# Performance work log

Measured on AMD Instinct MI355X. Metric: run time of the kernel, lower is better.

Reference implementation:

```python
import jax, jax.numpy as jnp
import numpy as np

B, T, E, H, O = 32, 512, 768, 3132, 19


def _ln(x, g, b, eps=1e-5):
    m = x.mean(-1, keepdims=True)
    v = x.var(-1, keepdims=True)
    return (x - m) / jnp.sqrt(v + eps) * g + b


def _cell(x, h, wih, bih, whh, bhh):
    # torch.nn.RNNCell with tanh nonlinearity
    return jnp.tanh(x @ wih.T + bih + h @ whh.T + bhh)


def _mha(seq, wqkv, bqkv, wo, bo):
    # seq: [T,B,D]; single-head torch MultiheadAttention (eval mode, no dropout)
    D = seq.shape[-1]
    qkv = seq @ wqkv.T + bqkv
    q, k, v = jnp.split(qkv, 3, axis=-1)
    scores = jnp.einsum('tbd,sbd->bts', q, k) / jnp.sqrt(jnp.asarray(D, seq.dtype))
    a = jax.nn.softmax(scores, axis=-1)
    ctx = jnp.einsum('bts,sbd->tbd', a, v)
    return ctx @ wo.T + bo


def setup_inputs() -> dict:
    key = jax.random.key(0)
    ks = jax.random.split(key, 12)
    s = lambda k, shape: jax.random.normal(k, shape, jnp.float32) * 0.02
    return {
        'x': jax.random.normal(ks[0], (B, T, E), jnp.float32),
        'in_g': jnp.ones((E,), jnp.float32), 'in_b': jnp.zeros((E,), jnp.float32),
        'w_ih1': s(ks[1], (H, E)), 'w_hh1': s(ks[2], (H, H)),
        'b_ih1': jnp.zeros((H,), jnp.float32), 'b_hh1': jnp.zeros((H,), jnp.float32),
        'ln1_g': jnp.ones((H,), jnp.float32), 'ln1_b': jnp.zeros((H,), jnp.float32),
        'w_ih2': s(ks[3], (E, H)), 'w_hh2': s(ks[4], (E, E)),
        'b_ih2': jnp.zeros((E,), jnp.float32), 'b_hh2': jnp.zeros((E,), jnp.float32),
        'mha1_wqkv': s(ks[5], (3 * H, H)), 'mha1_bqkv': jnp.zeros((3 * H,), jnp.float32),
        'mha1_wo': s(ks[6], (H, H)), 'mha1_bo': jnp.zeros((H,), jnp.float32),
        'mha2_wqkv': s(ks[7], (3 * E, E)), 'mha2_bqkv': jnp.zeros((3 * E,), jnp.float32),
        'mha2_wo': s(ks[8], (E, E)), 'mha2_bo': jnp.zeros((E,), jnp.float32),
        'w_cls': s(ks[9], (O, E)), 'b_cls': jnp.zeros((O,), jnp.float32),
    }


def reference(x, in_g, in_b, w_ih1, w_hh1, b_ih1, b_hh1, ln1_g, ln1_b,
              w_ih2, w_hh2, b_ih2, b_hh2,
              mha1_wqkv, mha1_bqkv, mha1_wo, mha1_bo,
              mha2_wqkv, mha2_bqkv, mha2_wo, mha2_bo, w_cls, b_cls):
    b = x.shape[0]
    xn = _ln(x, in_g, in_b)            # input_norm
    xs = jnp.swapaxes(xn, 0, 1)        # [T,B,E]
    h1_0 = jnp.zeros((b, w_ih1.shape[0]), x.dtype)
    h2_0 = jnp.zeros((b, w_ih2.shape[0]), x.dtype)

    def step(carry, xt):
        h1, h2 = carry
        h1 = _ln(_cell(xt, h1, w_ih1, b_ih1, w_hh1, b_hh1), ln1_g, ln1_b)
        h2 = _cell(h1, h2, w_ih2, b_ih2, w_hh2, b_hh2)
        return (h1, h2), (h1, h2)

    _, (h1s, h2s) = jax.lax.scan(step, (h1_0, h2_0), xs)  # [T,B,H], [T,B,E]
    ctx1 = _mha(h1s, mha1_wqkv, mha1_bqkv, mha1_wo, mha1_bo)  # dropout is identity in eval
    ctx2 = _mha(h2s, mha2_wqkv, mha2_bqkv, mha2_wo, mha2_bo)
    # the original second loop overwrites h1/h2 each t; only t = T-1 survives
    h1 = _cell(xs[-1], ctx1[-1], w_ih1, b_ih1, w_hh1, b_hh1)
    h2 = _cell(h1, ctx2[-1], w_ih2, b_ih2, w_hh2, b_hh2)
    return h2 @ w_cls.T + b_cls
```

## Files before the change

### kernel.cpp

```cpp
#include <hip/hip_runtime.h>
#include <cstdint>
#include <cmath>

#define BB 32
#define TT 512
#define EE 768
#define HH 3132
#define HP 3136
#define OO 19

#define NBLK 451
#define NTHR 256
#define WP 456
#define AP 232


#define PT(t) (((t) * 331) & 511)

typedef __attribute__((ext_vector_type(8))) short s8v;
typedef __attribute__((ext_vector_type(4))) float f4v;
typedef __attribute__((ext_vector_type(8))) unsigned short u16x8;

__device__ __forceinline__ unsigned short f2bf(float f) {
    uint32_t u = __float_as_uint(f);
    uint32_t r = u + 0x7FFFu + ((u >> 16) & 1u);
    return (unsigned short)(r >> 16);
}
__device__ __forceinline__ float bf2f(unsigned short h) {
    return __uint_as_float(((uint32_t)h) << 16);
}

#define MFMA(a, b, c) __builtin_amdgcn_mfma_f32_16x16x32_bf16((a), (b), (c), 0, 0, 0)

__device__ __forceinline__ f4v ld4_sc(const void* p) {
    f4v v;
    asm volatile("global_load_dwordx4 %0, %1, off sc0 sc1" : "=v"(v) : "v"(p) : "memory");
    return v;
}
#define WAITV() do { asm volatile("s_waitcnt vmcnt(0)" ::: "memory"); \
                     __builtin_amdgcn_sched_barrier(0); } while (0)
__device__ __forceinline__ void st_sc(float* p, float v) {
    __hip_atomic_store(p, v, __ATOMIC_RELAXED, __HIP_MEMORY_SCOPE_AGENT);
}
__device__ __forceinline__ void st16_sc(void* p, u16x8 v) {
    asm volatile("global_store_dwordx4 %0, %1, off sc0 sc1" :: "v"(p), "v"(v) : "memory");
}
__device__ __forceinline__ void st8_sc(void* p, uint2 v) {
    asm volatile("global_store_dwordx2 %0, %1, off sc0 sc1" :: "v"(p), "v"(v) : "memory");
}

struct PP {
    const unsigned short *xw1hi, *xw1lo;
    const unsigned short *whh1hi, *whh1lo, *wih2, *whh2;
    const float *b1c, *b2c, *gpad, *bepad;
    unsigned short *h1hist, *h2hist;
    unsigned short *h1nlo, *h2lo;
    float *part1, *part2;
    unsigned int *grp;
    unsigned int *epoch;
};

__device__ __forceinline__ void gbar(const PP& p, unsigned int k) {
    __syncthreads();
    asm volatile("s_waitcnt vmcnt(0)" ::: "memory");
    if (threadIdx.x == 0)
        __hip_atomic_fetch_add(&p.grp[(blockIdx.x & 63) * 32], 1u,
                               __ATOMIC_RELAXED, __HIP_MEMORY_SCOPE_AGENT);
    if (blockIdx.x == 0) {
        if (threadIdx.x < 64) {
            unsigned int mem = 7u + (threadIdx.x < (NBLK & 63) ? 1u : 0u);
            unsigned int tgt = mem * k;
            long g = 0;
            while (__hip_atomic_load(&p.grp[threadIdx.x * 32], __ATOMIC_RELAXED,
                                     __HIP_MEMORY_SCOPE_AGENT) < tgt) {
                __builtin_amdgcn_s_sleep(2);
                if (++g > (1L << 16)) break;
            }
        }
        __syncthreads();
        if (threadIdx.x == 0)
            __hip_atomic_store(p.epoch, k, __ATOMIC_RELAXED, __HIP_MEMORY_SCOPE_AGENT);
    } else {
        if (threadIdx.x == 0) {
            long g = 0;
            while (__hip_atomic_load(p.epoch, __ATOMIC_RELAXED,
                                     __HIP_MEMORY_SCOPE_AGENT) < k) {
                __builtin_amdgcn_s_sleep(2);
                if (++g > (1L << 16)) break;
            }
        }
    }
    __syncthreads();
    asm volatile("" ::: "memory");
}

__global__ __launch_bounds__(NTHR, 2) void persist_k(PP p) {
    __shared__ unsigned short Wlds[64][WP];
    __shared__ unsigned short Alds[32][AP];
    __shared__ float redS[4], redQ[4];
    const int blk = blockIdx.x, tid = threadIdx.x;
    const int wid = tid >> 6, lane = tid & 63;
    const int r = lane & 15, kg = lane >> 4;
    unsigned int bar = 0;

    const int t1nt = blk / 7,          t1ks = blk % 7;
    const int t2i  = blk - 343,        t2nt = t2i / 7, t2ks = t2i % 7;
    const int t3i  = blk - 427,        t3nt = t3i / 2, t3kh = t3i % 2;

    if (blk < 343) {
        const unsigned short* src = p.whh1hi + (size_t)(t1nt * 64) * HP + t1ks * 448;
        #pragma unroll
        for (int i = 0; i < 14; ++i) {
            int idx = tid + i * 256;
            int row = idx / 56, c8 = idx % 56;
            *(uint4*)&Wlds[row][c8 * 8] = *(const uint4*)(src + (size_t)row * HP + c8 * 8);
        }
    } else if (blk < 427) {
        const unsigned short* src = p.wih2 + (size_t)(t2nt * 64) * HP + t2ks * 448;
        #pragma unroll
        for (int i = 0; i < 14; ++i) {
            int idx = tid + i * 256;
            int row = idx / 56, c8 = idx % 56;
            *(uint4*)&Wlds[row][c8 * 8] = *(const uint4*)(src + (size_t)row * HP + c8 * 8);
        }
    } else {
        const unsigned short* src = p.whh2 + (size_t)(t3nt * 64) * EE + t3kh * 384;
        #pragma unroll
        for (int i = 0; i < 12; ++i) {
            int idx = tid + i * 256;
            int row = idx / 48, c8 = idx % 48;
            *(uint4*)&Wlds[row][c8 * 8] = *(const uint4*)(src + (size_t)row * EE + c8 * 8);
        }
    }
    __syncthreads();

    for (int t = 0; t <= TT; ++t) {
        if (blk < 343) {
            if (t >= 1 && t <= TT - 1) {
                f4v a0 = {0.f,0.f,0.f,0.f}, a1 = {0.f,0.f,0.f,0.f};
                const unsigned short* Wl = p.whh1lo + (size_t)(t1nt * 64 + wid * 16 + r) * HP + t1ks * 448 + kg * 8;
                const unsigned short* ringb = p.h1hist + (size_t)PT(t - 1) * BB * HP + t1ks * 448 + kg * 8;
                for (int hx = 0; hx < 2; ++hx) {
                    __syncthreads();
                    {
                        f4v lv[4];
                        #pragma unroll
                        for (int i = 0; i < 4; ++i) {
                            int idx = tid + i * 256;
                            int row = (idx < 896) ? idx / 28 : 0;
                            int c8  = (idx < 896) ? idx % 28 : 0;
                            lv[i] = ld4_sc(p.h1nlo + (size_t)row * HP + t1ks * 448 + hx * 224 + c8 * 8);
                        }
                        WAITV();
                        #pragma unroll
                        for (int i = 0; i < 4; ++i) {
                            int idx = tid + i * 256;
                            if (idx < 896) {
                                int row = idx / 28, c8 = idx % 28;
                                *(f4v*)&Alds[row][c8 * 8] = lv[i];
                            }
                        }
                    }
                    __syncthreads();
                    const unsigned short* Ah0 = ringb + (size_t)r * HP + hx * 224;
                    const unsigned short* Ah1 = ringb + (size_t)(r + 16) * HP + hx * 224;
                    const unsigned short* Wlh = Wl + hx * 224;
                    #pragma unroll
                    for (int kb = 0; kb < 7; ++kb) {
                        s8v bh  = *(const s8v*)&Wlds[wid * 16 + r][hx * 224 + kb * 32 + kg * 8];
                        s8v bl  = *(const s8v*)(Wlh + kb * 32);
                        s8v ah0 = *(const s8v*)(Ah0 + kb * 32);
                        s8v ah1 = *(const s8v*)(Ah1 + kb * 32);
                        s8v al0 = *(const s8v*)&Alds[r][kb * 32 + kg * 8];
                        s8v al1 = *(const s8v*)&Alds[r + 16][kb * 32 + kg * 8];
                        a0 = MFMA(ah0, bh, a0); a1 = MFMA(ah1, bh, a1);
                        a0 = MFMA(al0, bh, a0); a1 = MFMA(al1, bh, a1);
                        a0 = MFMA(ah0, bl, a0); a1 = MFMA(ah1, bl, a1);
                    }
                }
                int ncol = t1nt * 64 + wid * 16 + r;
                float* pp1 = p.part1 + (size_t)t1ks * BB * HP + ncol;
                #pragma unroll
                for (int q = 0; q < 4; ++q) {
                    st_sc(pp1 + (size_t)(kg * 4 + q) * HP,      a0[q]);
                    st_sc(pp1 + (size_t)(kg * 4 + q + 16) * HP, a1[q]);
                }
            }
        } else if (blk < 427) {
            if (t >= 1) {
                const unsigned short* ringb = p.h1hist + (size_t)PT(t - 1) * BB * HP + t2ks * 448 + kg * 8;
                const unsigned short* Ah0 = ringb + (size_t)r * HP;
                const unsigned short* Ah1 = ringb + (size_t)(r + 16) * HP;
                f4v a0 = {0.f,0.f,0.f,0.f}, a1 = {0.f,0.f,0.f,0.f};
                #pragma unroll
                for (int kb = 0; kb < 14; ++kb) {
                    s8v bh  = *(const s8v*)&Wlds[wid * 16 + r][kb * 32 + kg * 8];
                    s8v ah0 = *(const s8v*)(Ah0 + kb * 32);
                    s8v ah1 = *(const s8v*)(Ah1 + kb * 32);
                    a0 = MFMA(ah0, bh, a0); a1 = MFMA(ah1, bh, a1);
                }
                int ncol = t2nt * 64 + wid * 16 + r;
                float* pp2 = p.part2 + (size_t)t2ks * BB * EE + ncol;
                #pragma unroll
                for (int q = 0; q < 4; ++q) {
                    st_sc(pp2 + (size_t)(kg * 4 + q) * EE,      a0[q]);
                    st_sc(pp2 + (size_t)(kg * 4 + q + 16) * EE, a1[q]);
                }
            }
        } else {
            if (t >= 2) {
                const unsigned short* Hh = p.h2hist + (size_t)PT(t - 2) * BB * EE + t3kh * 384 + kg * 8;
                const unsigned short* Hl = p.h2lo + t3kh * 384 + kg * 8;
                f4v a0 = {0.f,0.f,0.f,0.f}, a1 = {0.f,0.f,0.f,0.f};
                #pragma unroll
                for (int c = 0; c < 2; ++c) {
                    f4v v0l[6], v1l[6];
                    #pragma unroll
                    for (int u = 0; u < 6; ++u) {
                        int kb = c * 6 + u;
                        v0l[u] = ld4_sc(Hl + (size_t)r * EE + kb * 32);
                        v1l[u] = ld4_sc(Hl + (size_t)(r + 16) * EE + kb * 32);
                    }
                    WAITV();
                    #pragma unroll
                    for (int u = 0; u < 6; ++u) {
                        int kb = c * 6 + u;
                        s8v bh  = *(const s8v*)&Wlds[wid * 16 + r][kb * 32 + kg * 8];
                        s8v ah0 = *(const s8v*)(Hh + (size_t)r * EE + kb * 32);
                        s8v ah1 = *(const s8v*)(Hh + (size_t)(r + 16) * EE + kb * 32);
                        a0 = MFMA(ah0, bh, a0);
                        a0 = MFMA(__builtin_bit_cast(s8v, v0l[u]), bh, a0);
                        a1 = MFMA(ah1, bh, a1);
                        a1 = MFMA(__builtin_bit_cast(s8v, v1l[u]), bh, a1);
                    }
                }
                int ncol = t3nt * 64 + wid * 16 + r;
                float* pp2 = p.part2 + (size_t)(7 + t3kh) * BB * EE + ncol;
                #pragma unroll
                for (int q = 0; q < 4; ++q) {
                    st_sc(pp2 + (size_t)(kg * 4 + q) * EE,      a0[q]);
                    st_sc(pp2 + (size_t)(kg * 4 + q + 16) * EE, a1[q]);
                }
            }
        }
        gbar(p, ++bar);

        if (blk < 32) {
            if (t <= TT - 1) {
                const int b = blk;
                const int nb = tid * 16;
                const bool act = (tid < 196);
                float acc[16];
                float s = 0.f, s2 = 0.f;
                if (act) {
                    #pragma unroll
                    for (int k4 = 0; k4 < 4; ++k4) {
                        f4v bb = *(const f4v*)(p.b1c + nb + k4 * 4);
                        #pragma unroll
                        for (int e = 0; e < 4; ++e) acc[k4 * 4 + e] = bb[e];
                    }
                    const u16x8* xh = (const u16x8*)(p.xw1hi + ((size_t)t * BB + b) * HP + nb);
                    const u16x8* xl = (const u16x8*)(p.xw1lo + ((size_t)t * BB + b) * HP + nb);
                    u16x8 h0v = xh[0], h1v = xh[1], l0v = xl[0], l1v = xl[1];
                    #pragma unroll
                    for (int j = 0; j < 8; ++j) acc[j]     += bf2f(h0v[j]) + bf2f(l0v[j]);
                    #pragma unroll
                    for (int j = 0; j < 8; ++j) acc[8 + j] += bf2f(h1v[j]) + bf2f(l1v[j]);
                    if (t > 0) {
                        {
                            f4v tmp[16];
                            #pragma unroll
                            for (int sl = 0; sl < 4; ++sl) {
                                const float* base = p.part1 + ((size_t)sl * BB + b) * HP + nb;
                                #pragma unroll
                                for (int k4 = 0; k4 < 4; ++k4) tmp[sl * 4 + k4] = ld4_sc(base + k4 * 4);
                            }
                            WAITV();
                            #pragma unroll
                            for (int sl = 0; sl < 4; ++sl)
                                #pragma unroll
                                for (int k4 = 0; k4 < 4; ++k4)
                                    #pragma unroll
                                    for (int e = 0; e < 4; ++e) acc[k4 * 4 + e] += tmp[sl * 4 + k4][e];
                        }
                        {
                            f4v tmp[12];
                            #pragma unroll
                            for (int sl = 0; sl < 3; ++sl) {
                                const float* base = p.part1 + ((size_t)(sl + 4) * BB + b) * HP + nb;
                                #pragma unroll
                                for (int k4 = 0; k4 < 4; ++k4) tmp[sl * 4 + k4] = ld4_sc(base + k4 * 4);
                            }
                            WAITV();
                            #pragma unroll
                            for (int sl = 0; sl < 3; ++sl)
                                #pragma unroll
                                for (int k4 = 0; k4 < 4; ++k4)
                                    #pragma unroll
                                    for (int e = 0; e < 4; ++e) acc[k4 * 4 + e] += tmp[sl * 4 + k4][e];
                        }
                    }
                    #pragma unroll
                    for (int j = 0; j < 16; ++j) {
                        if (nb + j < HH) {
                            float v = tanhf(acc[j]);
                            acc[j] = v; s += v; s2 += v * v;
                        } else acc[j] = 0.f;
                    }
                }
                for (int o = 32; o; o >>= 1) { s += __shfl_xor(s, o); s2 += __shfl_xor(s2, o); }
                if (lane == 0) { redS[wid] = s; redQ[wid] = s2; }
                __syncthreads();
                float S  = redS[0] + redS[1] + redS[2] + redS[3];
                float S2 = redQ[0] + redQ[1] + redQ[2] + redQ[3];
                float mm = S / (float)HH;
                float inv = rsqrtf(S2 / (float)HH - mm * mm + 1e-5f);
                __syncthreads();
                if (act) {
                    u16x8 ho0, ho1, lo0, lo1;
                    #pragma unroll
                    for (int k4 = 0; k4 < 4; ++k4) {
                        f4v gv = *(const f4v*)(p.gpad + nb + k4 * 4);
                        f4v bv = *(const f4v*)(p.bepad + nb + k4 * 4);
                        #pragma unroll
                        for (int e = 0; e < 4; ++e) {
                            int j = k4 * 4 + e, n = nb + j;
                            float o = (n < HH) ? (acc[j] - mm) * inv * gv[e] + bv[e] : 0.f;
                            unsigned short hb = f2bf(o);
                            unsigned short lb = f2bf(o - bf2f(hb));
                            if (j < 8) { ho0[j] = hb; lo0[j] = lb; }
                            else       { ho1[j - 8] = hb; lo1[j - 8] = lb; }
                        }
                    }
                    unsigned short* dh = p.h1hist + ((size_t)PT(t) * BB + b) * HP + nb;
                    unsigned short* dl = p.h1nlo + (size_t)b * HP + nb;
                    st16_sc(dh, ho0); st16_sc(dh + 8, ho1);
                    st16_sc(dl, lo0); st16_sc(dl + 8, lo1);
                }
            }
        } else if (blk < 64) {
            if (t >= 1) {
                const int b = blk - 32;
                if (tid < 192) {
                    const int nb = tid * 4;
                    f4v a4 = *(const f4v*)(p.b2c + nb);
                    f4v tp[9];
                    #pragma unroll
                    for (int sl = 0; sl < 9; ++sl)
                        tp[sl] = ld4_sc(p.part2 + ((size_t)sl * BB + b) * EE + nb);
                    WAITV();
                    #pragma unroll
                    for (int sl = 0; sl < 9; ++sl) {
                        float w = (t == 1 && sl >= 7) ? 0.f : 1.f;
                        #pragma unroll
                        for (int e = 0; e < 4; ++e) a4[e] += w * tp[sl][e];
                    }
                    unsigned short hb4[4], lb4[4];
                    #pragma unroll
                    for (int e = 0; e < 4; ++e) {
                        float v = tanhf(a4[e]);
                        hb4[e] = f2bf(v); lb4[e] = f2bf(v - bf2f(hb4[e]));
                    }
                    uint2 hp_, lp_;
                    hp_.x = (unsigned)hb4[0] | ((unsigned)hb4[1] << 16);
                    hp_.y = (unsigned)hb4[2] | ((unsigned)hb4[3] << 16);
                    lp_.x = (unsigned)lb4[0] | ((unsigned)lb4[1] << 16);
                    lp_.y = (unsigned)lb4[2] | ((unsigned)lb4[3] << 16);
                    st8_sc(p.h2hist + ((size_t)PT(t - 1) * BB + b) * EE + nb, hp_);
                    st8_sc(p.h2lo + (size_t)b * EE + nb, lp_);
                }
            }
        }
        gbar(p, ++bar);
    }
}

__global__ void ln_x_k(const float* __restrict__ x, const float* __restrict__ g,
                       const float* __restrict__ be, unsigned short* __restrict__ xnhi,
                       unsigned short* __restrict__ xnlo) {
    int bt = blockIdx.x;
    int b = bt >> 9, t = bt & 511;
    const float* row = x + ((size_t)b * TT + t) * EE;
    int tid = threadIdx.x;
    float v0 = row[tid], v1 = row[tid + 256], v2 = row[tid + 512];
    float s = v0 + v1 + v2, s2 = v0 * v0 + v1 * v1 + v2 * v2;
    for (int o = 32; o; o >>= 1) { s += __shfl_xor(s, o); s2 += __shfl_xor(s2, o); }
    __shared__ float r1[4], r2[4];
    int wid = tid >> 6, lane = tid & 63;
    if (lane == 0) { r1[wid] = s; r2[wid] = s2; }
    __syncthreads();
    s = r1[0] + r1[1] + r1[2] + r1[3];
    s2 = r2[0] + r2[1] + r2[2] + r2[3];
    float m = s / (float)EE, var = s2 / (float)EE - m * m;
    float inv = rsqrtf(var + 1e-5f);
    size_t ro = ((size_t)t * BB + b) * EE;
    float vals[3] = {v0, v1, v2};
#pragma unroll
    for (int i = 0; i < 3; i++) {
        int e = tid + i * 256;
        float o = (vals[i] - m) * inv * g[e] + be[e];
        unsigned short hb = f2bf(o);
        xnhi[ro + e] = hb;
        xnlo[ro + e] = f2bf(o - bf2f(hb));
    }
}

__global__ void castpad_k(const float* __restrict__ in, int N, int K,
                          unsigned short* __restrict__ out, int Np, int Kp) {
    size_t gid = (size_t)blockIdx.x * 256 + threadIdx.x;
    if (gid >= (size_t)Np * Kp) return;
    int n = (int)(gid / Kp), k = (int)(gid % Kp);
    out[gid] = (n < N && k < K) ? f2bf(in[(size_t)n * K + k]) : (unsigned short)0;
}

__global__ void castsplit_k(const float* __restrict__ in, int N, int K,
                            unsigned short* __restrict__ hi, unsigned short* __restrict__ lo,
                            int Np, int Kp) {
    size_t gid = (size_t)blockIdx.x * 256 + threadIdx.x;
    if (gid >= (size_t)Np * Kp) return;
    int n = (int)(gid / Kp), k = (int)(gid % Kp);
    float v = (n < N && k < K) ? in[(size_t)n * K + k] : 0.0f;
    unsigned short hb = f2bf(v);
    hi[gid] = hb;
    lo[gid] = f2bf(v - bf2f(hb));
}

__global__ void transcast_k(const float* __restrict__ in, int R, int C,
                            unsigned short* __restrict__ out, int Rp, int Cp) {
    __shared__ float tile[32][33];
    int c0 = blockIdx.x * 32, r0 = blockIdx.y * 32;
    int tx = threadIdx.x & 31, ty = threadIdx.x >> 5;
    for (int i = 0; i < 4; i++) {
        int r = r0 + ty + i * 8, c = c0 + tx;
        tile[ty + i * 8][tx] = (r < R && c < C) ? in[(size_t)r * C + c] : 0.0f;
    }
    __syncthreads();
    for (int i = 0; i < 4; i++) {
        int c = c0 + ty + i * 8, r = r0 + tx;
        if (c < Cp && r < Rp) out[(size_t)c * Rp + r] = f2bf(tile[tx][ty + i * 8]);
    }
}

__global__ void biascomb_k(const float* a, const float* b, float* o, int realN, int Np) {
    int gid = blockIdx.x * 256 + threadIdx.x;
    if (gid >= Np) return;
    o[gid] = (gid < realN) ? a[gid] + b[gid] : 0.0f;
}

__global__ void padcopy_k(const float* in, float* out, int realN, int Np) {
    int gid = blockIdx.x * 256 + threadIdx.x;
    if (gid >= Np) return;
    out[gid] = (gid < realN) ? in[gid] : 0.0f;
}

__global__ __launch_bounds__(256) void gemmbig_k(const unsigned short* __restrict__ Ahi,
                                                 const unsigned short* __restrict__ Alo,
                                                 const unsigned short* __restrict__ Whi,
                                                 const unsigned short* __restrict__ Wlo,
                                                 unsigned short* __restrict__ outhi,
                                                 unsigned short* __restrict__ outlo,
                                                 int Kld, int Np, int ksteps) {
    int m0 = blockIdx.x * 32;
    int n0 = blockIdx.y * 64;
    int wid = threadIdx.x >> 6, lane = threadIdx.x & 63;
    int r = lane & 15, kg = lane >> 4;
    size_t woff = (size_t)(n0 + wid * 16 + r) * Kld + kg * 8;
    const unsigned short* Whr = Whi + woff;
    const unsigned short* Wlr = Wlo + woff;
    size_t aoff = (size_t)(m0 + r) * Kld + kg * 8;
    const unsigned short* Ah0 = Ahi + aoff;
    const unsigned short* Ah1 = Ah0 + (size_t)16 * Kld;
    const unsigned short* Al0 = Alo + aoff;
    const unsigned short* Al1 = Al0 + (size_t)16 * Kld;
    f4v acc0 = {0.f, 0.f, 0.f, 0.f}, acc1 = {0.f, 0.f, 0.f, 0.f};
#pragma unroll 4
    for (int s = 0; s < ksteps; s++) {
        s8v bh  = *(const s8v*)(Whr + s * 32);
        s8v bl  = *(const s8v*)(Wlr + s * 32);
        s8v a0h = *(const s8v*)(Ah0 + s * 32);
        s8v a1h = *(const s8v*)(Ah1 + s * 32);
        s8v a0l = *(const s8v*)(Al0 + s * 32);
        s8v a1l = *(const s8v*)(Al1 + s * 32);
        acc0 = MFMA(a0h, bh, acc0); acc1 = MFMA(a1h, bh, acc1);
        acc0 = MFMA(a0l, bh, acc0); acc1 = MFMA(a1l, bh, acc1);
        acc0 = MFMA(a0h, bl, acc0); acc1 = MFMA(a1h, bl, acc1);
    }
    int ncol = n0 + wid * 16 + r;
#pragma unroll
    for (int q = 0; q < 4; q++) {
        int m = kg * 4 + q;
        float v0 = acc0[q], v1 = acc1[q];
        unsigned short h0 = f2bf(v0), h1 = f2bf(v1);
        outhi[(size_t)(m0 + m) * Np + ncol]      = h0;
        outlo[(size_t)(m0 + m) * Np + ncol]      = f2bf(v0 - bf2f(h0));
        outhi[(size_t)(m0 + m + 16) * Np + ncol] = h1;
        outlo[(size_t)(m0 + m + 16) * Np + ncol] = f2bf(v1 - bf2f(h1));
    }
}

__global__ __launch_bounds__(256) void gemm32_k(const unsigned short* __restrict__ A,
                                                const unsigned short* __restrict__ W,
                                                float* __restrict__ part,
                                                int Kld, int Np, int ksteps, int slot_base) {
    int n0 = blockIdx.x * 64;
    int kb = blockIdx.y;
    int k0 = kb * ksteps * 32;
    int wid = threadIdx.x >> 6, lane = threadIdx.x & 63;
    int r = lane & 15, kg = lane >> 4;
    const unsigned short* Wrow = W + (size_t)(n0 + wid * 16 + r) * Kld + k0 + kg * 8;
    const unsigned short* Ar0 = A + (size_t)r * Kld + k0 + kg * 8;
    const unsigned short* Ar1 = Ar0 + (size_t)16 * Kld;
    f4v acc0 = {0.f, 0.f, 0.f, 0.f}, acc1 = {0.f, 0.f, 0.f, 0.f};
#pragma unroll
    for (int s = 0; s < ksteps; s++) {
        s8v bf = *(const s8v*)(Wrow + s * 32);
        s8v a0 = *(const s8v*)(Ar0 + s * 32);
        s8v a1 = *(const s8v*)(Ar1 + s * 32);
        acc0 = MFMA(a0, bf, acc0);
        acc1 = MFMA(a1, bf, acc1);
    }
    int ncol = n0 + wid * 16 + r;
    float* p = part + (size_t)(slot_base + kb) * 32 * Np + ncol;
#pragma unroll
    for (int q = 0; q < 4; q++) {
        int m = kg * 4 + q;
        p[(size_t)m * Np]        = acc0[q];
        p[(size_t)(m + 16) * Np] = acc1[q];
    }
}

__global__ void epi_k(const float* __restrict__ part, int nslots, int Np, int realN,
                      const float* __restrict__ bias, int act,
                      unsigned short* __restrict__ outbf) {
    int gid = blockIdx.x * 256 + threadIdx.x;
    int b = gid / Np, n = gid % Np;
    float v = 0.0f;
    if (n < realN) {
        v = bias ? bias[n] : 0.0f;
        for (int s = 0; s < nslots; s++) v += part[(size_t)(s * 32 + b) * Np + n];
        if (act) v = tanhf(v);
    }
    outbf[(size_t)b * Np + n] = f2bf(v);
}

__global__ void qbk_k(const unsigned short* __restrict__ q, int Kp, int realK,
                      const float* __restrict__ bk, float* __restrict__ out) {
    int b = blockIdx.x, tid = threadIdx.x;
    float s = 0.f;
    for (int d = tid; d < realK; d += 256) s += bf2f(q[(size_t)b * Kp + d]) * bk[d];
    for (int o = 32; o; o >>= 1) s += __shfl_xor(s, o);
    __shared__ float r[4];
    if ((tid & 63) == 0) r[tid >> 6] = s;
// ... 66 lines not shown
    }
}

__global__ void fail_k(float* out) {
    int i = blockIdx.x * 256 + threadIdx.x;
    if (i < BB * OO) out[i] = 1e9f;
}

extern "C" void kernel_launch(void* const* d_in, const int* in_sizes, int n_in,
                              void* d_out, int out_size, void* d_ws, size_t ws_size,
                              hipStream_t stream) {
    const float* x        = (const float*)d_in[0];
    const float* in_g     = (const float*)d_in[1];
    const float* in_b     = (const float*)d_in[2];
    const float* w_ih1    = (const float*)d_in[3];
    const float* w_hh1    = (const float*)d_in[4];
    const float* b_ih1    = (const float*)d_in[5];
    const float* b_hh1    = (const float*)d_in[6];
    const float* ln1_g    = (const float*)d_in[7];
    const float* ln1_b    = (const float*)d_in[8];
    const float* w_ih2    = (const float*)d_in[9];
    const float* w_hh2    = (const float*)d_in[10];
    const float* b_ih2    = (const float*)d_in[11];
    const float* b_hh2    = (const float*)d_in[12];
    const float* m1_wqkv  = (const float*)d_in[13];
    const float* m1_bqkv  = (const float*)d_in[14];
    const float* m1_wo    = (const float*)d_in[15];
    const float* m1_bo    = (const float*)d_in[16];
    const float* m2_wqkv  = (const float*)d_in[17];
    const float* m2_bqkv  = (const float*)d_in[18];
    const float* m2_wo    = (const float*)d_in[19];
    const float* m2_bo    = (const float*)d_in[20];
    const float* w_cls    = (const float*)d_in[21];
    const float* b_cls    = (const float*)d_in[22];
    float* out = (float*)d_out;

    const size_t TB = (size_t)TT * BB;
    size_t cur = 0;
    auto alloc = [&](size_t bytes) { cur = (cur + 255) & ~(size_t)255; size_t o = cur; cur += bytes; return o; };
    char* ws = (char*)d_ws;
    #define US(off) ((unsigned short*)(ws + (off)))
    #define FP(off) ((float*)(ws + (off)))

    size_t o_xnhi   = alloc(TB * EE * 2);
    size_t o_xnlo   = alloc(TB * EE * 2);
    size_t o_wih1hi = alloc((size_t)HP * EE * 2);
    size_t o_wih1lo = alloc((size_t)HP * EE * 2);
    size_t o_whh1hi = alloc((size_t)HP * HP * 2);
    size_t o_whh1lo = alloc((size_t)HP * HP * 2);
    size_t o_wih2   = alloc((size_t)EE * HP * 2);
    size_t o_whh2   = alloc((size_t)EE * EE * 2);
    size_t o_h1s    = alloc(TB * HP * 2);
    size_t o_h2s    = alloc(TB * EE * 2);
    size_t o_h1nlo  = alloc((size_t)BB * HP * 2);
    size_t o_h2lo   = alloc((size_t)BB * EE * 2);
    size_t o_part1  = alloc((size_t)8 * BB * HP * 4);
    size_t o_part2  = alloc((size_t)9 * BB * EE * 4);
    size_t o_b1c    = alloc((size_t)HP * 4);
    size_t o_b2c    = alloc((size_t)EE * 4);
    size_t o_gpad   = alloc((size_t)HP * 4);
    size_t o_bepad  = alloc((size_t)HP * 4);
    size_t o_sync   = alloc(64 * 128 + 256);
    size_t o_xw1hi  = alloc(TB * HP * 2);
    size_t o_xw1lo  = alloc(TB * HP * 2);
    size_t o_q1     = alloc((size_t)BB * HP * 2);
    size_t o_qk1    = alloc((size_t)BB * HP * 2);
    size_t o_u1     = alloc((size_t)BB * HP * 2);
    size_t o_vc1    = alloc((size_t)BB * HP * 2);
    size_t o_ctx1   = alloc((size_t)BB * HP * 2);
    size_t o_qbk1   = alloc(BB * 4);
    size_t o_sc1    = alloc((size_t)BB * TT * 4);
    size_t o_aw1    = alloc((size_t)BB * TT * 4);
    size_t o_q2     = alloc((size_t)BB * EE * 2);
    size_t o_qk2    = alloc((size_t)BB * EE * 2);
    size_t o_u2     = alloc((size_t)BB * EE * 2);
    size_t o_vc2    = alloc((size_t)BB * EE * 2);
    size_t o_ctx2   = alloc((size_t)BB * EE * 2);
    size_t o_qbk2   = alloc(BB * 4);
    size_t o_sc2    = alloc((size_t)BB * TT * 4);
    size_t o_aw2    = alloc((size_t)BB * TT * 4);
    size_t o_h1f    = alloc((size_t)BB * HP * 2);
    size_t o_h2f    = alloc((size_t)BB * EE * 2);

    size_t ov = o_xw1hi;
    auto oalloc = [&](size_t bytes) { ov = (ov + 255) & ~(size_t)255; size_t o = ov; ov += bytes; return o; };
    size_t v_wq1  = oalloc((size_t)HP * HP * 2);
    size_t v_wk1T = oalloc((size_t)HP * HP * 2);
    size_t v_wv1  = oalloc((size_t)HP * HP * 2);
    size_t v_wo1  = oalloc((size_t)HP * HP * 2);
    size_t v_wq2  = oalloc((size_t)EE * EE * 2);
    size_t v_wk2T = oalloc((size_t)EE * EE * 2);
    size_t v_wv2  = oalloc((size_t)EE * EE * 2);
    size_t v_wo2  = oalloc((size_t)EE * EE * 2);

    if (ws_size < cur) {
        fail_k<<<3, 256, 0, stream>>>(out);
        return;
    }

    ln_x_k<<<BB * TT, 256, 0, stream>>>(x, in_g, in_b, US(o_xnhi), US(o_xnlo));
    castsplit_k<<<(HP * EE + 255) / 256, 256, 0, stream>>>(w_ih1, HH, EE, US(o_wih1hi), US(o_wih1lo), HP, EE);
    castsplit_k<<<(HP * HP + 255) / 256, 256, 0, stream>>>(w_hh1, HH, HH, US(o_whh1hi), US(o_whh1lo), HP, HP);
    castpad_k<<<(EE * HP + 255) / 256, 256, 0, stream>>>(w_ih2, EE, HH, US(o_wih2), EE, HP);
    castpad_k<<<(EE * EE + 255) / 256, 256, 0, stream>>>(w_hh2, EE, EE, US(o_whh2), EE, EE);
    biascomb_k<<<(HP + 255) / 256, 256, 0, stream>>>(b_ih1, b_hh1, FP(o_b1c), HH, HP);
    biascomb_k<<<(EE + 255) / 256, 256, 0, stream>>>(b_ih2, b_hh2, FP(o_b2c), EE, EE);
    padcopy_k<<<(HP + 255) / 256, 256, 0, stream>>>(ln1_g, FP(o_gpad), HH, HP);
    padcopy_k<<<(HP + 255) / 256, 256, 0, stream>>>(ln1_b, FP(o_bepad), HH, HP);
    hipMemsetAsync(ws + o_sync, 0, 64 * 128 + 256, stream);

    gemmbig_k<<<dim3((int)(TB / 32), HP / 64), 256, 0, stream>>>(US(o_xnhi), US(o_xnlo),
                                                                 US(o_wih1hi), US(o_wih1lo),
                                                                 US(o_xw1hi), US(o_xw1lo), EE, HP, EE / 32);

    PP pp;
    pp.xw1hi = US(o_xw1hi); pp.xw1lo = US(o_xw1lo);
    pp.whh1hi = US(o_whh1hi); pp.whh1lo = US(o_whh1lo);
    pp.wih2 = US(o_wih2); pp.whh2 = US(o_whh2);
    pp.b1c = FP(o_b1c); pp.b2c = FP(o_b2c);
    pp.gpad = FP(o_gpad); pp.bepad = FP(o_bepad);
    pp.h1hist = US(o_h1s); pp.h2hist = US(o_h2s);
    pp.h1nlo = US(o_h1nlo); pp.h2lo = US(o_h2lo);
    pp.part1 = FP(o_part1); pp.part2 = FP(o_part2);
    pp.grp = (unsigned int*)(ws + o_sync);
    pp.epoch = (unsigned int*)(ws + o_sync + 64 * 128);
    persist_k<<<NBLK, NTHR, 0, stream>>>(pp);

    castpad_k<<<(HP * HP + 255) / 256, 256, 0, stream>>>(m1_wqkv, HH, HH, US(v_wq1), HP, HP);
    castpad_k<<<(HP * HP + 255) / 256, 256, 0, stream>>>(m1_wqkv + (size_t)2 * HH * HH, HH, HH, US(v_wv1), HP, HP);
    castpad_k<<<(HP * HP + 255) / 256, 256, 0, stream>>>(m1_wo, HH, HH, US(v_wo1), HP, HP);
    transcast_k<<<dim3(HP / 32, HP / 32), 256, 0, stream>>>(m1_wqkv + (size_t)HH * HH, HH, HH, US(v_wk1T), HP, HP);
    castpad_k<<<(EE * EE + 255) / 256, 256, 0, stream>>>(m2_wqkv, EE, EE, US(v_wq2), EE, EE);
    castpad_k<<<(EE * EE + 255) / 256, 256, 0, stream>>>(m2_wqkv + (size_t)2 * EE * EE, EE, EE, US(v_wv2), EE, EE);
    castpad_k<<<(EE * EE + 255) / 256, 256, 0, stream>>>(m2_wo, EE, EE, US(v_wo2), EE, EE);
    transcast_k<<<dim3(EE / 32, EE / 32), 256, 0, stream>>>(m2_wqkv + (size_t)EE * EE, EE, EE, US(v_wk2T), EE, EE);

    const int PTLAST = (511 * 331) & 511;
    const unsigned short* h1last = US(o_h1s) + (size_t)PTLAST * BB * HP;
    const unsigned short* h2last = US(o_h2s) + (size_t)PTLAST * BB * EE;
    const float sc_scale1 = 1.0f / sqrtf((float)HH);
    const float sc_scale2 = 1.0f / sqrtf((float)EE);

    gemm32_k<<<dim3(HP / 64, 7), 256, 0, stream>>>(h1last, US(v_wq1), FP(o_part1), HP, HP, 14, 0);
    epi_k<<<BB * HP / 256, 256, 0, stream>>>(FP(o_part1), 7, HP, HH, m1_bqkv, 0, US(o_q1));
    gemm32_k<<<dim3(HP / 64, 7), 256, 0, stream>>>(US(o_q1), US(v_wk1T), FP(o_part1), HP, HP, 14, 0);
    epi_k<<<BB * HP / 256, 256, 0, stream>>>(FP(o_part1), 7, HP, HH, nullptr, 0, US(o_qk1));
    qbk_k<<<BB, 256, 0, stream>>>(US(o_q1), HP, HH, m1_bqkv + HH, FP(o_qbk1));
    scores_k<<<BB * TT / 4, 256, 0, stream>>>(US(o_h1s), US(o_qk1), FP(o_qbk1), FP(o_sc1), HP, sc_scale1);
    softmax_k<<<BB, 256, 0, stream>>>(FP(o_sc1), FP(o_aw1));
    attnsum_k<<<BB * HP / 256, 256, 0, stream>>>(US(o_h1s), FP(o_aw1), US(o_u1), HP);
    gemm32_k<<<dim3(HP / 64, 7), 256, 0, stream>>>(US(o_u1), US(v_wv1), FP(o_part1), HP, HP, 14, 0);
    epi_k<<<BB * HP / 256, 256, 0, stream>>>(FP(o_part1), 7, HP, HH, m1_bqkv + 2 * HH, 0, US(o_vc1));
    gemm32_k<<<dim3(HP / 64, 7), 256, 0, stream>>>(US(o_vc1), US(v_wo1), FP(o_part1), HP, HP, 14, 0);
    epi_k<<<BB * HP / 256, 256, 0, stream>>>(FP(o_part1), 7, HP, HH, m1_bo, 0, US(o_ctx1));

    gemm32_k<<<dim3(EE / 64, 3), 256, 0, stream>>>(h2last, US(v_wq2), FP(o_part2), EE, EE, 8, 0);
    epi_k<<<BB * EE / 256, 256, 0, stream>>>(FP(o_part2), 3, EE, EE, m2_bqkv, 0, US(o_q2));
    gemm32_k<<<dim3(EE / 64, 3), 256, 0, stream>>>(US(o_q2), US(v_wk2T), FP(o_part2), EE, EE, 8, 0);
    epi_k<<<BB * EE / 256, 256, 0, stream>>>(FP(o_part2), 3, EE, EE, nullptr, 0, US(o_qk2));
    qbk_k<<<BB, 256, 0, stream>>>(US(o_q2), EE, EE, m2_bqkv + EE, FP(o_qbk2));
    scores_k<<<BB * TT / 4, 256, 0, stream>>>(US(o_h2s), US(o_qk2), FP(o_qbk2), FP(o_sc2), EE, sc_scale2);
    softmax_k<<<BB, 256, 0, stream>>>(FP(o_sc2), FP(o_aw2));
    attnsum_k<<<BB * EE / 256, 256, 0, stream>>>(US(o_h2s), FP(o_aw2), US(o_u2), EE);
    gemm32_k<<<dim3(EE / 64, 3), 256, 0, stream>>>(US(o_u2), US(v_wv2), FP(o_part2), EE, EE, 8, 0);
    epi_k<<<BB * EE / 256, 256, 0, stream>>>(FP(o_part2), 3, EE, EE, m2_bqkv + 2 * EE, 0, US(o_vc2));
    gemm32_k<<<dim3(EE / 64, 3), 256, 0, stream>>>(US(o_vc2), US(v_wo2), FP(o_part2), EE, EE, 8, 0);
    epi_k<<<BB * EE / 256, 256, 0, stream>>>(FP(o_part2), 3, EE, EE, m2_bo, 0, US(o_ctx2));

    const unsigned short* xnlast = US(o_xnhi) + (size_t)(TT - 1) * BB * EE;
    gemm32_k<<<dim3(HP / 64, 1), 256, 0, stream>>>(xnlast, US(o_wih1hi), FP(o_part1), EE, HP, EE / 32, 0);
    gemm32_k<<<dim3(HP / 64, 7), 256, 0, stream>>>(US(o_ctx1), US(o_whh1hi), FP(o_part1), HP, HP, 14, 1);
    epi_k<<<BB * HP / 256, 256, 0, stream>>>(FP(o_part1), 8, HP, HH, FP(o_b1c), 1, US(o_h1f));
    gemm32_k<<<dim3(EE / 64, 7), 256, 0, stream>>>(US(o_h1f), US(o_wih2), FP(o_part2), HP, EE, 14, 0);
    gemm32_k<<<dim3(EE / 64, 1), 256, 0, stream>>>(US(o_ctx2), US(o_whh2), FP(o_part2), EE, EE, EE / 32, 7);
    epi_k<<<BB * EE / 256, 256, 0, stream>>>(FP(o_part2), 8, EE, EE, FP(o_b2c), 1, US(o_h2f));
// ... 3 lines not shown
```

Baseline: 17.82 ms.

## Fuse input projection into persistent RNN kernel and ring-buffer low-part hidden states

```diff
diff --git a/kernel.cpp b/kernel.cpp
--- a/kernel.cpp
+++ b/kernel.cpp
@@ -9,11 +9,13 @@
 #define HP 3136
 #define OO 19
 
-#define NBLK 451
+#define NBLK 500
 #define NTHR 256
 #define WP 456
-#define AP 232
-
+
+#define T1_END  343
+#define T1X_END 392
+#define T2_END  476
 
 #define PT(t) (((t) * 331) & 511)
 
@@ -32,13 +34,9 @@
 
 #define MFMA(a, b, c) __builtin_amdgcn_mfma_f32_16x16x32_bf16((a), (b), (c), 0, 0, 0)
 
-__device__ __forceinline__ f4v ld4_sc(const void* p) {
-    f4v v;
-    asm volatile("global_load_dwordx4 %0, %1, off sc0 sc1" : "=v"(v) : "v"(p) : "memory");
-    return v;
-}
-#define WAITV() do { asm volatile("s_waitcnt vmcnt(0)" ::: "memory"); \
-                     __builtin_amdgcn_sched_barrier(0); } while (0)
+__device__ __forceinline__ float ldf_sc(const float* p) {
+    return __hip_atomic_load(p, __ATOMIC_RELAXED, __HIP_MEMORY_SCOPE_AGENT);
+}
 __device__ __forceinline__ void st_sc(float* p, float v) {
     __hip_atomic_store(p, v, __ATOMIC_RELAXED, __HIP_MEMORY_SCOPE_AGENT);
 }
@@ -50,11 +48,12 @@
 }
 
 struct PP {
-    const unsigned short *xw1hi, *xw1lo;
+    const unsigned short *xnhi, *xnlo;
+    const unsigned short *wih1hi, *wih1lo;
     const unsigned short *whh1hi, *whh1lo, *wih2, *whh2;
     const float *b1c, *b2c, *gpad, *bepad;
     unsigned short *h1hist, *h2hist;
-    unsigned short *h1nlo, *h2lo;
+    unsigned short *h1lring, *h2lring;
     float *part1, *part2;
     unsigned int *grp;
     unsigned int *epoch;
@@ -78,12 +77,13 @@
             }
         }
         __syncthreads();
-        if (threadIdx.x == 0)
-            __hip_atomic_store(p.epoch, k, __ATOMIC_RELAXED, __HIP_MEMORY_SCOPE_AGENT);
+        if (threadIdx.x < 64)
+            __hip_atomic_store(&p.epoch[threadIdx.x * 32], k,
+                               __ATOMIC_RELAXED, __HIP_MEMORY_SCOPE_AGENT);
     } else {
         if (threadIdx.x == 0) {
             long g = 0;
-            while (__hip_atomic_load(p.epoch, __ATOMIC_RELAXED,
+            while (__hip_atomic_load(&p.epoch[(blockIdx.x & 63) * 32], __ATOMIC_RELAXED,
                                      __HIP_MEMORY_SCOPE_AGENT) < k) {
                 __builtin_amdgcn_s_sleep(2);
                 if (++g > (1L << 16)) break;
@@ -96,18 +96,18 @@
 
 __global__ __launch_bounds__(NTHR, 2) void persist_k(PP p) {
     __shared__ unsigned short Wlds[64][WP];
-    __shared__ unsigned short Alds[32][AP];
     __shared__ float redS[4], redQ[4];
     const int blk = blockIdx.x, tid = threadIdx.x;
     const int wid = tid >> 6, lane = tid & 63;
     const int r = lane & 15, kg = lane >> 4;
     unsigned int bar = 0;
 
-    const int t1nt = blk / 7,          t1ks = blk % 7;
-    const int t2i  = blk - 343,        t2nt = t2i / 7, t2ks = t2i % 7;
-    const int t3i  = blk - 427,        t3nt = t3i / 2, t3kh = t3i % 2;
-
-    if (blk < 343) {
+    const int t1nt = blk / 7,           t1ks = blk % 7;
+    const int t1xnt = blk - T1_END;
+    const int t2i  = blk - T1X_END,     t2nt = t2i / 7, t2ks = t2i % 7;
+    const int t3i  = blk - T2_END,      t3nt = t3i / 2, t3kh = t3i % 2;
+
+    if (blk < T1_END) {
         const unsigned short* src = p.whh1hi + (size_t)(t1nt * 64) * HP + t1ks * 448;
         #pragma unroll
         for (int i = 0; i < 14; ++i) {
@@ -115,7 +115,7 @@
             int row = idx / 56, c8 = idx % 56;
             *(uint4*)&Wlds[row][c8 * 8] = *(const uint4*)(src + (size_t)row * HP + c8 * 8);
         }
-    } else if (blk < 427) {
+    } else if (blk >= T1X_END && blk < T2_END) {
         const unsigned short* src = p.wih2 + (size_t)(t2nt * 64) * HP + t2ks * 448;
         #pragma unroll
         for (int i = 0; i < 14; ++i) {
@@ -123,7 +123,7 @@
             int row = idx / 56, c8 = idx % 56;
             *(uint4*)&Wlds[row][c8 * 8] = *(const uint4*)(src + (size_t)row * HP + c8 * 8);
         }
-    } else {
+    } else if (blk >= T2_END) {
         const unsigned short* src = p.whh2 + (size_t)(t3nt * 64) * EE + t3kh * 384;
         #pragma unroll
         for (int i = 0; i < 12; ++i) {
@@ -135,48 +135,23 @@
     __syncthreads();
 
     for (int t = 0; t <= TT; ++t) {
-        if (blk < 343) {
+        if (blk < T1_END) {
             if (t >= 1 && t <= TT - 1) {
+                const unsigned short* rh = p.h1hist  + (size_t)PT(t - 1) * BB * HP + t1ks * 448 + kg * 8;
+                const unsigned short* rl = p.h1lring + (size_t)PT(t - 1) * BB * HP + t1ks * 448 + kg * 8;
+                const unsigned short* Wl = p.whh1lo + (size_t)(t1nt * 64 + wid * 16 + r) * HP + t1ks * 448 + kg * 8;
                 f4v a0 = {0.f,0.f,0.f,0.f}, a1 = {0.f,0.f,0.f,0.f};
-                const unsigned short* Wl = p.whh1lo + (size_t)(t1nt * 64 + wid * 16 + r) * HP + t1ks * 448 + kg * 8;
-                const unsigned short* ringb = p.h1hist + (size_t)PT(t - 1) * BB * HP + t1ks * 448 + kg * 8;
-                for (int hx = 0; hx < 2; ++hx) {
-                    __syncthreads();
-                    {
-                        f4v lv[4];
-                        #pragma unroll
-                        for (int i = 0; i < 4; ++i) {
-                            int idx = tid + i * 256;
-                            int row = (idx < 896) ? idx / 28 : 0;
-                            int c8  = (idx < 896) ? idx % 28 : 0;
-                            lv[i] = ld4_sc(p.h1nlo + (size_t)row * HP + t1ks * 448 + hx * 224 + c8 * 8);
-                        }
-                        WAITV();
-                        #pragma unroll
-                        for (int i = 0; i < 4; ++i) {
-                            int idx = tid + i * 256;
-                            if (idx < 896) {
-                                int row = idx / 28, c8 = idx % 28;
-                                *(f4v*)&Alds[row][c8 * 8] = lv[i];
-                            }
-                        }
-                    }
-                    __syncthreads();
-                    const unsigned short* Ah0 = ringb + (size_t)r * HP + hx * 224;
-                    const unsigned short* Ah1 = ringb + (size_t)(r + 16) * HP + hx * 224;
-                    const unsigned short* Wlh = Wl + hx * 224;
-                    #pragma unroll
-                    for (int kb = 0; kb < 7; ++kb) {
-                        s8v bh  = *(const s8v*)&Wlds[wid * 16 + r][hx * 224 + kb * 32 + kg * 8];
-                        s8v bl  = *(const s8v*)(Wlh + kb * 32);
-                        s8v ah0 = *(const s8v*)(Ah0 + kb * 32);
-                        s8v ah1 = *(const s8v*)(Ah1 + kb * 32);
-                        s8v al0 = *(const s8v*)&Alds[r][kb * 32 + kg * 8];
-                        s8v al1 = *(const s8v*)&Alds[r + 16][kb * 32 + kg * 8];
-                        a0 = MFMA(ah0, bh, a0); a1 = MFMA(ah1, bh, a1);
-                        a0 = MFMA(al0, bh, a0); a1 = MFMA(al1, bh, a1);
-                        a0 = MFMA(ah0, bl, a0); a1 = MFMA(ah1, bl, a1);
-                    }
+                #pragma unroll
+                for (int kb = 0; kb < 14; ++kb) {
+                    s8v bh  = *(const s8v*)&Wlds[wid * 16 + r][kb * 32 + kg * 8];
+                    s8v bl  = *(const s8v*)(Wl + kb * 32);
+                    s8v ah0 = *(const s8v*)(rh + (size_t)r * HP + kb * 32);
+                    s8v ah1 = *(const s8v*)(rh + (size_t)(r + 16) * HP + kb * 32);
+                    s8v al0 = *(const s8v*)(rl + (size_t)r * HP + kb * 32);
+                    s8v al1 = *(const s8v*)(rl + (size_t)(r + 16) * HP + kb * 32);
+                    a0 = MFMA(ah0, bh, a0); a1 = MFMA(ah1, bh, a1);
+                    a0 = MFMA(al0, bh, a0); a1 = MFMA(al1, bh, a1);
+                    a0 = MFMA(ah0, bl, a0); a1 = MFMA(ah1, bl, a1);
                 }
                 int ncol = t1nt * 64 + wid * 16 + r;
                 float* pp1 = p.part1 + (size_t)t1ks * BB * HP + ncol;
@@ -186,7 +161,37 @@
                     st_sc(pp1 + (size_t)(kg * 4 + q + 16) * HP, a1[q]);
                 }
             }
-        } else if (blk < 427) {
+        } else if (blk < T1X_END) {
+            if (t <= TT - 1) {
+                int n0 = t1xnt * 64;
+                const unsigned short* A0h = p.xnhi + ((size_t)t * BB + r) * EE + kg * 8;
+                const unsigned short* A1h = A0h + (size_t)16 * EE;
+                const unsigned short* A0l = p.xnlo + ((size_t)t * BB + r) * EE + kg * 8;
+                const unsigned short* A1l = A0l + (size_t)16 * EE;
+                const unsigned short* Whr = p.wih1hi + (size_t)(n0 + wid * 16 + r) * EE + kg * 8;
+                const unsigned short* Wlr = p.wih1lo + (size_t)(n0 + wid * 16 + r) * EE + kg * 8;
+                f4v a0 = {0.f,0.f,0.f,0.f}, a1 = {0.f,0.f,0.f,0.f};
+                #pragma unroll 6
+                for (int s = 0; s < 24; ++s) {
+                    s8v bh  = *(const s8v*)(Whr + s * 32);
+                    s8v bl  = *(const s8v*)(Wlr + s * 32);
+                    s8v a0h = *(const s8v*)(A0h + s * 32);
+                    s8v a1h = *(const s8v*)(A1h + s * 32);
+                    s8v a0l = *(const s8v*)(A0l + s * 32);
+                    s8v a1l = *(const s8v*)(A1l + s * 32);
+                    a0 = MFMA(a0h, bh, a0); a1 = MFMA(a1h, bh, a1);
+                    a0 = MFMA(a0l, bh, a0); a1 = MFMA(a1l, bh, a1);
+                    a0 = MFMA(a0h, bl, a0); a1 = MFMA(a1h, bl, a1);
+                }
+                int ncol = n0 + wid * 16 + r;
+                float* pp1 = p.part1 + (size_t)7 * BB * HP + ncol;
+                #pragma unroll
+                for (int q = 0; q < 4; ++q) {
+                    st_sc(pp1 + (size_t)(kg * 4 + q) * HP,      a0[q]);
+                    st_sc(pp1 + (size_t)(kg * 4 + q + 16) * HP, a1[q]);
+                }
+            }
+        } else if (blk < T2_END) {
             if (t >= 1) {
                 const unsigned short* ringb = p.h1hist + (size_t)PT(t - 1) * BB * HP + t2ks * 448 + kg * 8;
                 const unsigned short* Ah0 = ringb + (size_t)r * HP;
@@ -209,30 +214,18 @@
             }
         } else {
             if (t >= 2) {
-                const unsigned short* Hh = p.h2hist + (size_t)PT(t - 2) * BB * EE + t3kh * 384 + kg * 8;
-                const unsigned short* Hl = p.h2lo + t3kh * 384 + kg * 8;
+                const unsigned short* Hh = p.h2hist  + (size_t)PT(t - 2) * BB * EE + t3kh * 384 + kg * 8;
+                const unsigned short* Hl = p.h2lring + (size_t)PT(t - 2) * BB * EE + t3kh * 384 + kg * 8;
                 f4v a0 = {0.f,0.f,0.f,0.f}, a1 = {0.f,0.f,0.f,0.f};
                 #pragma unroll
-                for (int c = 0; c < 2; ++c) {
-                    f4v v0l[6], v1l[6];
-                    #pragma unroll
-                    for (int u = 0; u < 6; ++u) {
-                        int kb = c * 6 + u;
-                        v0l[u] = ld4_sc(Hl + (size_t)r * EE + kb * 32);
-                        v1l[u] = ld4_sc(Hl + (size_t)(r + 16) * EE + kb * 32);
-                    }
-                    WAITV();
-                    #pragma unroll
-                    for (int u = 0; u < 6; ++u) {
-                        int kb = c * 6 + u;
-                        s8v bh  = *(const s8v*)&Wlds[wid * 16 + r][kb * 32 + kg * 8];
-                        s8v ah0 = *(const s8v*)(Hh + (size_t)r * EE + kb * 32);
-                        s8v ah1 = *(const s8v*)(Hh + (size_t)(r + 16) * EE + kb * 32);
-                        a0 = MFMA(ah0, bh, a0);
-                        a0 = MFMA(__builtin_bit_cast(s8v, v0l[u]), bh, a0);
-                        a1 = MFMA(ah1, bh, a1);
-                        a1 = MFMA(__builtin_bit_cast(s8v, v1l[u]), bh, a1);
-                    }
+                for (int kb = 0; kb < 12; ++kb) {
+                    s8v bh  = *(const s8v*)&Wlds[wid * 16 + r][kb * 32 + kg * 8];
+                    s8v ah0 = *(const s8v*)(Hh + (size_t)r * EE + kb * 32);
+                    s8v ah1 = *(const s8v*)(Hh + (size_t)(r + 16) * EE + kb * 32);
+                    s8v al0 = *(const s8v*)(Hl + (size_t)r * EE + kb * 32);
+                    s8v al1 = *(const s8v*)(Hl + (size_t)(r + 16) * EE + kb * 32);
+                    a0 = MFMA(ah0, bh, a0); a0 = MFMA(al0, bh, a0);
+                    a1 = MFMA(ah1, bh, a1); a1 = MFMA(al1, bh, a1);
                 }
                 int ncol = t3nt * 64 + wid * 16 + r;
                 float* pp2 = p.part2 + (size_t)(7 + t3kh) * BB * EE + ncol;
@@ -259,46 +252,11 @@
                         #pragma unroll
                         for (int e = 0; e < 4; ++e) acc[k4 * 4 + e] = bb[e];
                     }
-                    const u16x8* xh = (const u16x8*)(p.xw1hi + ((size_t)t * BB + b) * HP + nb);
-                    const u16x8* xl = (const u16x8*)(p.xw1lo + ((size_t)t * BB + b) * HP + nb);
-                    u16x8 h0v = xh[0], h1v = xh[1], l0v = xl[0], l1v = xl[1];
                     #pragma unroll
-                    for (int j = 0; j < 8; ++j) acc[j]     += bf2f(h0v[j]) + bf2f(l0v[j]);
-                    #pragma unroll
-                    for (int j = 0; j < 8; ++j) acc[8 + j] += bf2f(h1v[j]) + bf2f(l1v[j]);
-                    if (t > 0) {
-                        {
-                            f4v tmp[16];
-                            #pragma unroll
-                            for (int sl = 0; sl < 4; ++sl) {
-                                const float* base = p.part1 + ((size_t)sl * BB + b) * HP + nb;
-                                #pragma unroll
-                                for (int k4 = 0; k4 < 4; ++k4) tmp[sl * 4 + k4] = ld4_sc(base + k4 * 4);
-                            }
-                            WAITV();
-                            #pragma unroll
-                            for (int sl = 0; sl < 4; ++sl)
-                                #pragma unroll
-                                for (int k4 = 0; k4 < 4; ++k4)
-                                    #pragma unroll
-                                    for (int e = 0; e < 4; ++e) acc[k4 * 4 + e] += tmp[sl * 4 + k4][e];
-                        }
-                        {
-                            f4v tmp[12];
-                            #pragma unroll
-                            for (int sl = 0; sl < 3; ++sl) {
-                                const float* base = p.part1 + ((size_t)(sl + 4) * BB + b) * HP + nb;
-                                #pragma unroll
-                                for (int k4 = 0; k4 < 4; ++k4) tmp[sl * 4 + k4] = ld4_sc(base + k4 * 4);
-                            }
-                            WAITV();
-                            #pragma unroll
-                            for (int sl = 0; sl < 3; ++sl)
-                                #pragma unroll
-                                for (int k4 = 0; k4 < 4; ++k4)
-                                    #pragma unroll
-                                    for (int e = 0; e < 4; ++e) acc[k4 * 4 + e] += tmp[sl * 4 + k4][e];
-                        }
+                    for (int sl = 0; sl < 8; ++sl) {
+                        const float* base = p.part1 + ((size_t)sl * BB + b) * HP + nb;
+                        #pragma unroll
+                        for (int j = 0; j < 16; ++j) acc[j] += ldf_sc(base + j);
                     }
                     #pragma unroll
                     for (int j = 0; j < 16; ++j) {
@@ -332,8 +290,8 @@
                             else       { ho1[j - 8] = hb; lo1[j - 8] = lb; }
                         }
                     }
-                    unsigned short* dh = p.h1hist + ((size_t)PT(t) * BB + b) * HP + nb;
-                    unsigned short* dl = p.h1nlo + (size_t)b * HP + nb;
+                    unsigned short* dh = p.h1hist  + ((size_t)PT(t) * BB + b) * HP + nb;
+                    unsigned short* dl = p.h1lring + ((size_t)PT(t) * BB + b) * HP + nb;
                     st16_sc(dh, ho0); st16_sc(dh + 8, ho1);
                     st16_sc(dl, lo0); st16_sc(dl + 8, lo1);
                 }
@@ -344,16 +302,11 @@
                 if (tid < 192) {
                     const int nb = tid * 4;
                     f4v a4 = *(const f4v*)(p.b2c + nb);
-                    f4v tp[9];
-                    #pragma unroll
-                    for (int sl = 0; sl < 9; ++sl)
-                        tp[sl] = ld4_sc(p.part2 + ((size_t)sl * BB + b) * EE + nb);
-                    WAITV();
                     #pragma unroll
                     for (int sl = 0; sl < 9; ++sl) {
-                        float w = (t == 1 && sl >= 7) ? 0.f : 1.f;
+                        const float* base = p.part2 + ((size_t)sl * BB + b) * EE + nb;
                         #pragma unroll
-                        for (int e = 0; e < 4; ++e) a4[e] += w * tp[sl][e];
+                        for (int e = 0; e < 4; ++e) a4[e] += ldf_sc(base + e);
                     }
                     unsigned short hb4[4], lb4[4];
                     #pragma unroll
@@ -366,8 +319,8 @@
                     hp_.y = (unsigned)hb4[2] | ((unsigned)hb4[3] << 16);
                     lp_.x = (unsigned)lb4[0] | ((unsigned)lb4[1] << 16);
                     lp_.y = (unsigned)lb4[2] | ((unsigned)lb4[3] << 16);
-                    st8_sc(p.h2hist + ((size_t)PT(t - 1) * BB + b) * EE + nb, hp_);
-                    st8_sc(p.h2lo + (size_t)b * EE + nb, lp_);
+                    st8_sc(p.h2hist  + ((size_t)PT(t - 1) * BB + b) * EE + nb, hp_);
+                    st8_sc(p.h2lring + ((size_t)PT(t - 1) * BB + b) * EE + nb, lp_);
                 }
             }
         }
@@ -453,51 +406,6 @@
     out[gid] = (gid < realN) ? in[gid] : 0.0f;
 }
 
-__global__ __launch_bounds__(256) void gemmbig_k(const unsigned short* __restrict__ Ahi,
-                                                 const unsigned short* __restrict__ Alo,
-                                                 const unsigned short* __restrict__ Whi,
-                                                 const unsigned short* __restrict__ Wlo,
-                                                 unsigned short* __restrict__ outhi,
-                                                 unsigned short* __restrict__ outlo,
-                                                 int Kld, int Np, int ksteps) {
-    int m0 = blockIdx.x * 32;
-    int n0 = blockIdx.y * 64;
-    int wid = threadIdx.x >> 6, lane = threadIdx.x & 63;
-    int r = lane & 15, kg = lane >> 4;
-    size_t woff = (size_t)(n0 + wid * 16 + r) * Kld + kg * 8;
-    const unsigned short* Whr = Whi + woff;
-    const unsigned short* Wlr = Wlo + woff;
-    size_t aoff = (size_t)(m0 + r) * Kld + kg * 8;
-    const unsigned short* Ah0 = Ahi + aoff;
-    const unsigned short* Ah1 = Ah0 + (size_t)16 * Kld;
-    const unsigned short* Al0 = Alo + aoff;
-    const unsigned short* Al1 = Al0 + (size_t)16 * Kld;
-    f4v acc0 = {0.f, 0.f, 0.f, 0.f}, acc1 = {0.f, 0.f, 0.f, 0.f};
-#pragma unroll 4
-    for (int s = 0; s < ksteps; s++) {
-        s8v bh  = *(const s8v*)(Whr + s * 32);
-        s8v bl  = *(const s8v*)(Wlr + s * 32);
-        s8v a0h = *(const s8v*)(Ah0 + s * 32);
-        s8v a1h = *(const s8v*)(Ah1 + s * 32);
-        s8v a0l = *(const s8v*)(Al0 + s * 32);
-        s8v a1l = *(const s8v*)(Al1 + s * 32);
-        acc0 = MFMA(a0h, bh, acc0); acc1 = MFMA(a1h, bh, acc1);
-        acc0 = MFMA(a0l, bh, acc0); acc1 = MFMA(a1l, bh, acc1);
-        acc0 = MFMA(a0h, bl, acc0); acc1 = MFMA(a1h, bl, acc1);
-    }
-    int ncol = n0 + wid * 16 + r;
-#pragma unroll
-    for (int q = 0; q < 4; q++) {
-        int m = kg * 4 + q;
-        float v0 = acc0[q], v1 = acc1[q];
-        unsigned short h0 = f2bf(v0), h1 = f2bf(v1);
-        outhi[(size_t)(m0 + m) * Np + ncol]      = h0;
-        outlo[(size_t)(m0 + m) * Np + ncol]      = f2bf(v0 - bf2f(h0));
-        outhi[(size_t)(m0 + m + 16) * Np + ncol] = h1;
-        outlo[(size_t)(m0 + m + 16) * Np + ncol] = f2bf(v1 - bf2f(h1));
-    }
-}
-
 __global__ __launch_bounds__(256) void gemm32_k(const unsigned short* __restrict__ A,
                                                 const unsigned short* __restrict__ W,
                                                 float* __restrict__ part,
@@ -670,17 +578,15 @@
     size_t o_whh2   = alloc((size_t)EE * EE * 2);
     size_t o_h1s    = alloc(TB * HP * 2);
     size_t o_h2s    = alloc(TB * EE * 2);
-    size_t o_h1nlo  = alloc((size_t)BB * HP * 2);
-    size_t o_h2lo   = alloc((size_t)BB * EE * 2);
+    size_t o_h1lr   = alloc(TB * HP * 2);
+    size_t o_h2lr   = alloc(TB * EE * 2);
     size_t o_part1  = alloc((size_t)8 * BB * HP * 4);
     size_t o_part2  = alloc((size_t)9 * BB * EE * 4);
     size_t o_b1c    = alloc((size_t)HP * 4);
     size_t o_b2c    = alloc((size_t)EE * 4);
     size_t o_gpad   = alloc((size_t)HP * 4);
     size_t o_bepad  = alloc((size_t)HP * 4);
-    size_t o_sync   = alloc(64 * 128 + 256);
-    size_t o_xw1hi  = alloc(TB * HP * 2);
-    size_t o_xw1lo  = alloc(TB * HP * 2);
+    size_t o_sync   = alloc(64 * 128 * 2 + 256);
     size_t o_q1     = alloc((size_t)BB * HP * 2);
     size_t o_qk1    = alloc((size_t)BB * HP * 2);
     size_t o_u1     = alloc((size_t)BB * HP * 2);
@@ -700,7 +606,7 @@
     size_t o_h1f    = alloc((size_t)BB * HP * 2);
     size_t o_h2f    = alloc((size_t)BB * EE * 2);
 
-    size_t ov = o_xw1hi;
+    size_t ov = o_h1lr;
     auto oalloc = [&](size_t bytes) { ov = (ov + 255) & ~(size_t)255; size_t o = ov; ov += bytes; return o; };
     size_t v_wq1  = oalloc((size_t)HP * HP * 2);
     size_t v_wk1T = oalloc((size_t)HP * HP * 2);
@@ -725,20 +631,19 @@
     biascomb_k<<<(EE + 255) / 256, 256, 0, stream>>>(b_ih2, b_hh2, FP(o_b2c), EE, EE);
     padcopy_k<<<(HP + 255) / 256, 256, 0, stream>>>(ln1_g, FP(o_gpad), HH, HP);
     padcopy_k<<<(HP + 255) / 256, 256, 0, stream>>>(ln1_b, FP(o_bepad), HH, HP);
-    hipMemsetAsync(ws + o_sync, 0, 64 * 128 + 256, stream);
-
-    gemmbig_k<<<dim3((int)(TB / 32), HP / 64), 256, 0, stream>>>(US(o_xnhi), US(o_xnlo),
-                                                                 US(o_wih1hi), US(o_wih1lo),
-                                                                 US(o_xw1hi), US(o_xw1lo), EE, HP, EE / 32);
+    hipMemsetAsync(ws + o_sync, 0, 64 * 128 * 2 + 256, stream);
+    hipMemsetAsync(ws + o_part1, 0, (size_t)8 * BB * HP * 4, stream);
+    hipMemsetAsync(ws + o_part2, 0, (size_t)9 * BB * EE * 4, stream);
 
     PP pp;
-    pp.xw1hi = US(o_xw1hi); pp.xw1lo = US(o_xw1lo);
+    pp.xnhi = US(o_xnhi); pp.xnlo = US(o_xnlo);
+    pp.wih1hi = US(o_wih1hi); pp.wih1lo = US(o_wih1lo);
     pp.whh1hi = US(o_whh1hi); pp.whh1lo = US(o_whh1lo);
     pp.wih2 = US(o_wih2); pp.whh2 = US(o_whh2);
     pp.b1c = FP(o_b1c); pp.b2c = FP(o_b2c);
     pp.gpad = FP(o_gpad); pp.bepad = FP(o_bepad);
     pp.h1hist = US(o_h1s); pp.h2hist = US(o_h2s);
-    pp.h1nlo = US(o_h1nlo); pp.h2lo = US(o_h2lo);
+    pp.h1lring = US(o_h1lr); pp.h2lring = US(o_h2lr);
     pp.part1 = FP(o_part1); pp.part2 = FP(o_part2);
     pp.grp = (unsigned int*)(ws + o_sync);
     pp.epoch = (unsigned int*)(ws + o_sync + 64 * 128);
```

After: 38.98 ms. 119% more time.
